# Performance work log

Hardware: AMD Instinct MI355X
Metric: run time of the kernel (lower is better)

The kernel has to match this reference:

```python
import jax, jax.numpy as jnp
import numpy as np

V, D, B, T, S, NH, DFF, NL, PAD = 4096, 512, 32, 32, 8, 8, 2048, 4, 0


def _ln(x, g, b, eps=1e-5):
    m = jnp.mean(x, -1, keepdims=True)
    v = jnp.mean((x - m) ** 2, -1, keepdims=True)
    return (x - m) * jax.lax.rsqrt(v + eps) * g + b


def _mha(q, k, v, in_w, in_b, out_w, out_b, attn_mask=None, kpm=None):
    b_, lq, d = q.shape
    lk = k.shape[1]
    dh = d // NH
    wq, wk, wv = jnp.split(in_w, 3, 0)
    bq, bk, bv = jnp.split(in_b, 3)
    qh = (q @ wq.T + bq).reshape(b_, lq, NH, dh).transpose(0, 2, 1, 3)
    kh = (k @ wk.T + bk).reshape(b_, lk, NH, dh).transpose(0, 2, 1, 3)
    vh = (v @ wv.T + bv).reshape(b_, lk, NH, dh).transpose(0, 2, 1, 3)
    s = jnp.einsum('bhqd,bhkd->bhqk', qh, kh) * (1.0 / np.sqrt(dh))
    if attn_mask is not None:
        s = jnp.where(attn_mask[None, None], -1e9, s)
    if kpm is not None:
        s = jnp.where(kpm[:, None, None, :], -1e9, s)
    a = jax.nn.softmax(s, -1)
    o = jnp.einsum('bhqk,bhkd->bhqd', a, vh).transpose(0, 2, 1, 3).reshape(b_, lq, d)
    return o @ out_w.T + out_b


def setup_inputs():
    key = jax.random.key(0)
    ks = iter(jax.random.split(key, 48))
    nrm = lambda shape, s=0.02: jax.random.normal(next(ks), shape, jnp.float32) * s
    d = {}
    d['input_ids'] = jax.random.randint(next(ks), (B, T), 1, V)
    d['ego_info'] = jax.random.normal(next(ks), (B, 3), jnp.float32)
    d['agent_tokens'] = jax.random.randint(next(ks), (B, T, S), 1, V)
    d['agent_feats'] = jax.random.normal(next(ks), (B, T, S, 5), jnp.float32)
    d['goal'] = jax.random.randint(next(ks), (B,), 1, V)
    d['emb'] = nrm((V, D), 1.0).at[PAD].set(0.0)  # padding_idx row zeroed
    d['se_w1'] = nrm((D, D + 3)); d['se_b1'] = jnp.zeros(D)
    d['se_w2'] = nrm((D, D)); d['se_b2'] = jnp.zeros(D)
    d['be_w1'] = nrm((D, D + 5)); d['be_b1'] = jnp.zeros(D)
    d['be_w2'] = nrm((D, D)); d['be_b2'] = jnp.zeros(D)
    for nm in ('in', 'mem', 'outn'):
        d[nm + '_g'] = jnp.ones(D); d[nm + '_b'] = jnp.zeros(D)
    d['sa_in_w'] = nrm((NL, 3 * D, D)); d['sa_in_b'] = jnp.zeros((NL, 3 * D))
    d['sa_out_w'] = nrm((NL, D, D)); d['sa_out_b'] = jnp.zeros((NL, D))
    d['ca_in_w'] = nrm((NL, 3 * D, D)); d['ca_in_b'] = jnp.zeros((NL, 3 * D))
    d['ca_out_w'] = nrm((NL, D, D)); d['ca_out_b'] = jnp.zeros((NL, D))
    d['ff_w1'] = nrm((NL, DFF, D)); d['ff_b1'] = jnp.zeros((NL, DFF))
    d['ff_w2'] = nrm((NL, D, DFF)); d['ff_b2'] = jnp.zeros((NL, D))
    for nm in ('ln1', 'ln2', 'ln3'):
        d[nm + '_g'] = jnp.ones((NL, D)); d[nm + '_b'] = jnp.zeros((NL, D))
    d['proj_w'] = nrm((V, D)); d['proj_b'] = jnp.zeros(V)
    return d


def _forward(input_ids, agent_tokens, goal, ego_info, agent_feats, emb, se_w1, se_b1, se_w2, se_b2, be_w1, be_b1, be_w2, be_b2, in_g, in_b, mem_g, mem_b, outn_g, outn_b, sa_in_w, sa_in_b, sa_out_w, sa_out_b, ca_in_w, ca_in_b, ca_out_w, ca_out_b, ff_w1, ff_b1, ff_w2, ff_b2, ln1_g, ln1_b, ln2_g, ln2_b, ln3_g, ln3_b, proj_w, proj_b):
    # --- encode_self_state: embed + fuse ego features -> (B, T, D) ---
    tok = emb[input_ids]
    ego = jnp.broadcast_to(ego_info[:, None, :], (B, T, 3))
    fused = jax.nn.relu(jnp.concatenate([tok, ego], -1) @ se_w1.T + se_b1) @ se_w2.T + se_b2
    self_state = _ln(fused, in_g, in_b)
    # --- encode_agent_topology -> env (B, T, S+1, D) ---
    amask = agent_tokens != -1
    aemb = emb[jnp.where(amask, agent_tokens, PAD)]
    astate = jax.nn.relu(jnp.concatenate([aemb, agent_feats], -1) @ be_w1.T + be_b1) @ be_w2.T + be_b2
    astate = astate * amask[..., None]
    goal_e = jnp.broadcast_to(emb[goal][:, None, None, :], (B, T, 1, D))
    env = _ln(jnp.concatenate([astate, goal_e], 2), mem_g, mem_b)
    # --- windowed memory for each step t in [1, T): frames [t-2, t-1, t] clipped ---
    steps = jnp.arange(1, T)
    idx = jnp.clip(steps[:, None] + jnp.array([-2, -1, 0]), 0, T - 1)  # (T-1, 3)
    mems = env[:, idx].reshape(B, T - 1, 3 * (S + 1), D).transpose(1, 0, 2, 3)  # (T-1, B, 3A, D)
    causal = jnp.triu(jnp.ones((T, T), bool), 1)
    kpm = input_ids == PAD

    # One full-length causal decoder run per step (vmapped); identical math to the
    # original prefix loop since position t only sees keys <= t, and we read position t.
    def decode(mem):
        x = self_state
        for l in range(NL):
            x = _ln(x + _mha(x, x, x, sa_in_w[l], sa_in_b[l], sa_out_w[l], sa_out_b[l], causal, kpm), ln1_g[l], ln1_b[l])
            x = _ln(x + _mha(x, mem, mem, ca_in_w[l], ca_in_b[l], ca_out_w[l], ca_out_b[l]), ln2_g[l], ln2_b[l])
            ff = jax.nn.relu(x @ ff_w1[l].T + ff_b1[l]) @ ff_w2[l].T + ff_b2[l]
            x = _ln(x + ff, ln3_g[l], ln3_b[l])
        return x

    dec_all = jax.vmap(decode)(mems)  # (T-1, B, T, D)
    sel = dec_all[jnp.arange(T - 1), :, steps, :]  # (T-1, B, D): last position of each prefix
    logits = _ln(sel, outn_g, outn_b) @ proj_w.T + proj_b
    return jnp.transpose(logits, (1, 0, 2))  # (B, T-1, V)


def reference(input_ids, ego_info, agent_tokens, agent_feats, goal, emb, se_w1, se_b1, se_w2, se_b2, be_w1, be_b1, be_w2, be_b2, in_g, in_b, mem_g, mem_b, outn_g, outn_b, sa_in_w, sa_in_b, sa_out_w, sa_out_b, ca_in_w, ca_in_b, ca_out_w, ca_out_b, ff_w1, ff_b1, ff_w2, ff_b2, ln1_g, ln1_b, ln2_g, ln2_b, ln3_g, ln3_b, proj_w, proj_b):
    return _forward(input_ids, agent_tokens, goal, ego_info, agent_feats, emb, se_w1, se_b1, se_w2, se_b2, be_w1, be_b1, be_w2, be_b2, in_g, in_b, mem_g, mem_b, outn_g, outn_b, sa_in_w, sa_in_b, sa_out_w, sa_out_b, ca_in_w, ca_in_b, ca_out_w, ca_out_b, ff_w1, ff_b1, ff_w2, ff_b2, ln1_g, ln1_b, ln2_g, ln2_b, ln3_g, ln3_b, proj_w, proj_b)
```

## Files before the change

### kernel.cpp

```cpp
#include <hip/hip_runtime.h>
#include <hip/hip_bf16.h>
#include <stdint.h>

typedef __hip_bfloat16 bf16;
typedef __attribute__((ext_vector_type(8))) short bf16x8;
typedef __attribute__((ext_vector_type(4))) float f32x4;

__device__ __forceinline__ float b2f(bf16 v) { return __bfloat162float(v); }
__device__ __forceinline__ bf16 f2b(float v) { return __float2bfloat16(v); }
__device__ __forceinline__ unsigned short f2bu(float v) {
    bf16 h = __float2bfloat16(v);
    return *(unsigned short*)&h;
}
__device__ __forceinline__ short f2bs(float v) {
    bf16 h = __float2bfloat16(v);
    return *(short*)&h;
}
__device__ __forceinline__ float su2f(unsigned short u) {
    unsigned int x = ((unsigned int)u) << 16;
    return *(float*)&x;
}

__device__ __forceinline__ void gload_lds16(const void* g, void* l) {
    __builtin_amdgcn_global_load_lds((const __attribute__((address_space(1))) void*)g,
                                     (__attribute__((address_space(3))) void*)l, 16, 0, 0);
}

__device__ __forceinline__ int swz_byte(int row, int kk) {
    return row * 80 + 2 * (kk & 7) + 16 * ((kk >> 3) ^ (row & 3));
}

__global__ __launch_bounds__(256) void mfma_gemm(
    const bf16* __restrict__ A, const bf16* __restrict__ W,
    const float* __restrict__ bias, void* __restrict__ C,
    int M, int N, int K, int c_bf16, int relu, int store_mode)
{
    __shared__ bf16 As[128 * 64];
    __shared__ bf16 Bs[128 * 64];
    const int gx = gridDim.x;
    const int nwg = gx * gridDim.y;
    const int orig = blockIdx.y * gx + blockIdx.x;
    const int qq = nwg >> 3, rr8 = nwg & 7;
    const int xcd = orig & 7, lid = orig >> 3;
    const int wgid = (xcd < rr8 ? xcd * (qq + 1) : rr8 * (qq + 1) + (xcd - rr8) * qq) + lid;
    const int m0 = (wgid / gx) * 128, n0 = (wgid % gx) * 128;

    const int tid = threadIdx.x;
    const int wave = tid >> 6, lane = tid & 63;
    const int wr = wave >> 1, wc = wave & 1;
    const int fr = lane & 15, fg = lane >> 4;
    f32x4 acc[4][4] = {};

    const int srow = lane >> 3;
    const int sunit = (lane & 7) ^ srow;

    for (int k0 = 0; k0 < K; k0 += 64) {
#pragma unroll
        for (int c = 0; c < 4; ++c) {
            const int chunk = wave * 4 + c;
            const int arow = m0 + chunk * 8 + srow;
            const int brow = n0 + chunk * 8 + srow;
            gload_lds16(A + (size_t)arow * K + k0 + sunit * 8, (char*)As + chunk * 1024);
            gload_lds16(W + (size_t)brow * K + k0 + sunit * 8, (char*)Bs + chunk * 1024);
        }
        __syncthreads();
#pragma unroll
        for (int kk = 0; kk < 64; kk += 32) {
            bf16x8 af[4], bw[4];
            const int bo = (kk + fg * 8) * 2;
#pragma unroll
            for (int t = 0; t < 4; ++t) {
                const int ra = wr * 64 + t * 16 + fr;
                af[t] = *(const bf16x8*)((const char*)As + ra * 128 + (bo ^ ((ra & 7) << 4)));
                const int rb = wc * 64 + t * 16 + fr;
                bw[t] = *(const bf16x8*)((const char*)Bs + rb * 128 + (bo ^ ((rb & 7) << 4)));
            }
#pragma unroll
            for (int mt = 0; mt < 4; ++mt)
#pragma unroll
                for (int nt = 0; nt < 4; ++nt)
                    acc[mt][nt] = __builtin_amdgcn_mfma_f32_16x16x32_bf16(
                        af[mt], bw[nt], acc[mt][nt], 0, 0, 0);
        }
        __syncthreads();
    }
#pragma unroll
    for (int mt = 0; mt < 4; ++mt) {
#pragma unroll
        for (int r = 0; r < 4; ++r) {
            const int m = m0 + wr * 64 + mt * 16 + fg * 4 + r;
            if (m >= M) continue;
            size_t orow = (size_t)m;
            if (store_mode == 1) orow = (size_t)(m & 31) * 31 + (m >> 5);
#pragma unroll
            for (int nt = 0; nt < 4; ++nt) {
                const int n = n0 + wc * 64 + nt * 16 + fr;
                float v = acc[mt][nt][r] + bias[n];
                if (relu) v = fmaxf(v, 0.f);
                if (c_bf16) ((bf16*)C)[orow * N + n] = f2b(v);
                else        ((float*)C)[orow * N + n] = v;
            }
        }
    }
}

__global__ __launch_bounds__(256) void self_attn_mfma(
    const bf16* __restrict__ qkv, const int* __restrict__ input_ids,
    bf16* __restrict__ attn_out)
{
    const int bid = blockIdx.x;
    const int hp = bid & 3;
    const int mb = bid >> 2;
    const int b = mb & 31;
    const size_t rowbase = (size_t)mb * 32;

    __shared__ __align__(16) char vt_raw[2][64 * 80];
    __shared__ __align__(16) char ps_raw[4][16 * 80];
    __shared__ float kpmv[32];

    const int tid = threadIdx.x;
    {
        const int r = tid & 31, u = tid >> 5;
#pragma unroll
        for (int e2 = 0; e2 < 2; ++e2) {
            const int h = hp * 2 + e2;
            bf16x8 v8 = *(const bf16x8*)(qkv + (rowbase + r) * 1536 + 1024 + h * 64 + u * 8);
#pragma unroll
            for (int j = 0; j < 8; ++j)
                *(short*)(vt_raw[e2] + swz_byte(u * 8 + j, r)) = v8[j];
        }
    }
    if (tid < 32) kpmv[tid] = (input_ids[b * 32 + tid] == 0) ? -1e9f : 0.f;
    __syncthreads();

    const int wave = tid >> 6, lane = tid & 63;
    const int e = wave >> 1;
    const int h = hp * 2 + e;
    const int qi = wave & 1;
    const int c = lane & 15, fg = lane >> 4;

    const bf16* qrow = qkv + (rowbase + qi * 16 + c) * 1536 + h * 64;
    bf16x8 af0 = *(const bf16x8*)(qrow + fg * 8);
    bf16x8 af1 = *(const bf16x8*)(qrow + 32 + fg * 8);
    f32x4 s[2];
#pragma unroll
    for (int kj = 0; kj < 2; ++kj) {
        const bf16* krow = qkv + (rowbase + kj * 16 + c) * 1536 + 512 + h * 64;
        bf16x8 b0 = *(const bf16x8*)(krow + fg * 8);
        bf16x8 b1 = *(const bf16x8*)(krow + 32 + fg * 8);
        f32x4 a = {};
        a = __builtin_amdgcn_mfma_f32_16x16x32_bf16(af0, b0, a, 0, 0, 0);
        a = __builtin_amdgcn_mfma_f32_16x16x32_bf16(af1, b1, a, 0, 0, 0);
        s[kj] = a;
    }

#pragma unroll
    for (int r = 0; r < 4; ++r) {
        const int qg = qi * 16 + fg * 4 + r;
        float v0 = s[0][r] * 0.125f + kpmv[c];
        float v1 = s[1][r] * 0.125f + kpmv[16 + c];
        if (c > qg) v0 = -1e9f;
        if (16 + c > qg) v1 = -1e9f;
        float m = fmaxf(v0, v1);
        m = fmaxf(m, __shfl_xor(m, 1)); m = fmaxf(m, __shfl_xor(m, 2));
        m = fmaxf(m, __shfl_xor(m, 4)); m = fmaxf(m, __shfl_xor(m, 8));
        float e0 = __expf(v0 - m), e1 = __expf(v1 - m);
        float sm = e0 + e1;
        sm += __shfl_xor(sm, 1); sm += __shfl_xor(sm, 2);
        sm += __shfl_xor(sm, 4); sm += __shfl_xor(sm, 8);
        float inv = 1.f / sm;
        *(short*)(ps_raw[wave] + swz_byte(fg * 4 + r, c))      = f2bs(e0 * inv);
        *(short*)(ps_raw[wave] + swz_byte(fg * 4 + r, 16 + c)) = f2bs(e1 * inv);
    }

    bf16x8 pa = *(const bf16x8*)(ps_raw[wave] + c * 80 + 16 * (fg ^ (c & 3)));
    f32x4 o[4];
#pragma unroll
    for (int dj = 0; dj < 4; ++dj) {
        bf16x8 bv = *(const bf16x8*)(vt_raw[e] + (dj * 16 + c) * 80 + 16 * (fg ^ (c & 3)));
        f32x4 a = {};
        o[dj] = __builtin_amdgcn_mfma_f32_16x16x32_bf16(pa, bv, a, 0, 0, 0);
    }
#pragma unroll
    for (int dj = 0; dj < 4; ++dj)
#pragma unroll
        for (int r = 0; r < 4; ++r)
            attn_out[(rowbase + qi * 16 + fg * 4 + r) * 512 + h * 64 + dj * 16 + c] = f2b(o[dj][r]);
}

__global__ __launch_bounds__(256) void cross_attn_mfma(
    const bf16* __restrict__ q, int qshared, const bf16* __restrict__ kv,
    bf16* __restrict__ attn_out)
{
    const int bid = blockIdx.x;
    const int hp = bid & 3;
    const int mb = bid >> 2;
    const size_t qb = (size_t)(qshared ? (mb & 31) : mb) * 32;
    const size_t kvb = (size_t)mb * 27;
    const size_t ob = (size_t)mb * 32;

    __shared__ __align__(16) char vt_raw[2][64 * 80];
    __shared__ __align__(16) char ps_raw[4][16 * 80];

    const int tid = threadIdx.x;
    {
        const int r = tid & 31, u = tid >> 5;
#pragma unroll
        for (int e2 = 0; e2 < 2; ++e2) {
            const int h = hp * 2 + e2;
            bf16x8 v8 = *(const bf16x8*)(kv + (kvb + r) * 1024 + 512 + h * 64 + u * 8);
#pragma unroll
            for (int j = 0; j < 8; ++j)
                *(short*)(vt_raw[e2] + swz_byte(u * 8 + j, r)) = v8[j];
        }
    }
    __syncthreads();

    const int wave = tid >> 6, lane = tid & 63;
    const int e = wave >> 1;
    const int h = hp * 2 + e;
    const int qi = wave & 1;
    const int c = lane & 15, fg = lane >> 4;

    const bf16* qrow = q + (qb + qi * 16 + c) * 512 + h * 64;
    bf16x8 af0 = *(const bf16x8*)(qrow + fg * 8);
    bf16x8 af1 = *(const bf16x8*)(qrow + 32 + fg * 8);
    f32x4 s[2];
#pragma unroll
    for (int kj = 0; kj < 2; ++kj) {
        const bf16* krow = kv + (kvb + kj * 16 + c) * 1024 + h * 64;
        bf16x8 b0 = *(const bf16x8*)(krow + fg * 8);
        bf16x8 b1 = *(const bf16x8*)(krow + 32 + fg * 8);
        f32x4 a = {};
        a = __builtin_amdgcn_mfma_f32_16x16x32_bf16(af0, b0, a, 0, 0, 0);
        a = __builtin_amdgcn_mfma_f32_16x16x32_bf16(af1, b1, a, 0, 0, 0);
        s[kj] = a;
    }
#pragma unroll
    for (int r = 0; r < 4; ++r) {
        float v0 = s[0][r] * 0.125f;
        float v1 = (16 + c < 27) ? s[1][r] * 0.125f : -1e9f;
        float m = fmaxf(v0, v1);
        m = fmaxf(m, __shfl_xor(m, 1)); m = fmaxf(m, __shfl_xor(m, 2));
        m = fmaxf(m, __shfl_xor(m, 4)); m = fmaxf(m, __shfl_xor(m, 8));
        float e0 = __expf(v0 - m), e1 = __expf(v1 - m);
        float sm = e0 + e1;
        sm += __shfl_xor(sm, 1); sm += __shfl_xor(sm, 2);
        sm += __shfl_xor(sm, 4); sm += __shfl_xor(sm, 8);
        float inv = 1.f / sm;
        *(short*)(ps_raw[wave] + swz_byte(fg * 4 + r, c))      = f2bs(e0 * inv);
        *(short*)(ps_raw[wave] + swz_byte(fg * 4 + r, 16 + c)) = f2bs(e1 * inv);
    }
    bf16x8 pa = *(const bf16x8*)(ps_raw[wave] + c * 80 + 16 * (fg ^ (c & 3)));
    f32x4 o[4];
#pragma unroll
    for (int dj = 0; dj < 4; ++dj) {
        bf16x8 bv = *(const bf16x8*)(vt_raw[e] + (dj * 16 + c) * 80 + 16 * (fg ^ (c & 3)));
        f32x4 a = {};
        o[dj] = __builtin_amdgcn_mfma_f32_16x16x32_bf16(pa, bv, a, 0, 0, 0);
    }
#pragma unroll
    for (int dj = 0; dj < 4; ++dj)
#pragma unroll
        for (int r = 0; r < 4; ++r)
            attn_out[(ob + qi * 16 + fg * 4 + r) * 512 + h * 64 + dj * 16 + c] = f2b(o[dj][r]);
}

__global__ __launch_bounds__(256) void ln_kernel(
    const float* __restrict__ x, const float* __restrict__ g,
    const float* __restrict__ b_, float* __restrict__ outf,
    bf16* __restrict__ outb, int rows)
{
    int row = blockIdx.x * 4 + (threadIdx.x >> 6);
    if (row >= rows) return;
    int lane = threadIdx.x & 63;
    const float4* xr = (const float4*)(x + (size_t)row * 512);
    float4 v[2];
    float sum = 0.f;
#pragma unroll
    for (int j = 0; j < 2; ++j) {
        v[j] = xr[lane + 64 * j];
        sum += v[j].x + v[j].y + v[j].z + v[j].w;
    }
    for (int o = 32; o; o >>= 1) sum += __shfl_xor(sum, o, 64);
    float mean = sum * (1.f / 512.f);
    float vs = 0.f;
#pragma unroll
    for (int j = 0; j < 2; ++j) {
        float dx = v[j].x - mean, dy = v[j].y - mean, dz = v[j].z - mean, dw = v[j].w - mean;
        vs += dx * dx + dy * dy + dz * dz + dw * dw;
    }
    for (int o = 32; o; o >>= 1) vs += __shfl_xor(vs, o, 64);
    float rstd = rsqrtf(vs * (1.f / 512.f) + 1e-5f);
#pragma unroll
    for (int j = 0; j < 2; ++j) {
        int u = lane + 64 * j;
        float4 g4 = ((const float4*)g)[u];
        float4 b4 = ((const float4*)b_)[u];
        float4 o4;
        o4.x = (v[j].x - mean) * rstd * g4.x + b4.x;
        o4.y = (v[j].y - mean) * rstd * g4.y + b4.y;
        o4.z = (v[j].z - mean) * rstd * g4.z + b4.z;
        o4.w = (v[j].w - mean) * rstd * g4.w + b4.w;
        if (outf) ((float4*)(outf + (size_t)row * 512))[u] = o4;
        if (outb) {
            ushort4 s4 = { f2bu(o4.x), f2bu(o4.y), f2bu(o4.z), f2bu(o4.w) };
            ((ushort4*)(outb + (size_t)row * 512))[u] = s4;
        }
    }
}

__global__ __launch_bounds__(256) void ln_res2_kernel(
    const float* __restrict__ xin, int rowmask, const bf16* __restrict__ br,
    const float* __restrict__ g, const float* __restrict__ b_,
    float* __restrict__ xout, bf16* __restrict__ xbout, int rows)
{
    int row = blockIdx.x * 4 + (threadIdx.x >> 6);
    if (row >= rows) return;
    int lane = threadIdx.x & 63;
    const float4* xr = (const float4*)(xin + (size_t)(row & rowmask) * 512);
    const ushort4* brr = (const ushort4*)(br + (size_t)row * 512);
    float4 v[2];
    float sum = 0.f;
#pragma unroll
    for (int j = 0; j < 2; ++j) {
        int u = lane + 64 * j;
        float4 a = xr[u];
        ushort4 s4 = brr[u];
        a.x += su2f(s4.x); a.y += su2f(s4.y); a.z += su2f(s4.z); a.w += su2f(s4.w);
        v[j] = a;
        sum += a.x + a.y + a.z + a.w;
    }
    for (int o = 32; o; o >>= 1) sum += __shfl_xor(sum, o, 64);
    float mean = sum * (1.f / 512.f);
    float vs = 0.f;
#pragma unroll
    for (int j = 0; j < 2; ++j) {
        float dx = v[j].x - mean, dy = v[j].y - mean, dz = v[j].z - mean, dw = v[j].w - mean;
        vs += dx * dx + dy * dy + dz * dz + dw * dw;
    }
    for (int o = 32; o; o >>= 1) vs += __shfl_xor(vs, o, 64);
    float rstd = rsqrtf(vs * (1.f / 512.f) + 1e-5f);
#pragma unroll
    for (int j = 0; j < 2; ++j) {
        int u = lane + 64 * j;
        float4 g4 = ((const float4*)g)[u];
        float4 b4 = ((const float4*)b_)[u];
        float4 o4;
        o4.x = (v[j].x - mean) * rstd * g4.x + b4.x;
        o4.y = (v[j].y - mean) * rstd * g4.y + b4.y;
        o4.z = (v[j].z - mean) * rstd * g4.z + b4.z;
        o4.w = (v[j].w - mean) * rstd * g4.w + b4.w;
        ((float4*)(xout + (size_t)row * 512))[u] = o4;
        ushort4 s4 = { f2bu(o4.x), f2bu(o4.y), f2bu(o4.z), f2bu(o4.w) };
        ((ushort4*)(xbout + (size_t)row * 512))[u] = s4;
    }
}

__global__ __launch_bounds__(256) void env_ln_kernel(
    const float* __restrict__ astate, const int* __restrict__ atok,
    const float* __restrict__ emb, const int* __restrict__ goal,
    const float* __restrict__ g, const float* __restrict__ b_, float* __restrict__ env)
{
    int row = blockIdx.x * 4 + (threadIdx.x >> 6);
    if (row >= 9216) return;
    int lane = threadIdx.x & 63;
    int s9 = row % 9;
    int bt = row / 9;
    float4 v[2];
    if (s9 < 8) {
        int ar = bt * 8 + s9;
        float msk = (atok[ar] != -1) ? 1.f : 0.f;
#pragma unroll
        for (int j = 0; j < 2; ++j) {
            float4 a = ((const float4*)(astate + (size_t)ar * 512))[lane + 64 * j];
            a.x *= msk; a.y *= msk; a.z *= msk; a.w *= msk;
            v[j] = a;
        }
    } else {
        int gi = goal[bt >> 5];
#pragma unroll
        for (int j = 0; j < 2; ++j)
            v[j] = ((const float4*)(emb + (size_t)gi * 512))[lane + 64 * j];
    }
    float sum = 0.f;
#pragma unroll
    for (int j = 0; j < 2; ++j) sum += v[j].x + v[j].y + v[j].z + v[j].w;
    for (int o = 32; o; o >>= 1) sum += __shfl_xor(sum, o, 64);
    float mean = sum * (1.f / 512.f);
    float vs = 0.f;
#pragma unroll
    for (int j = 0; j < 2; ++j) {
        float dx = v[j].x - mean, dy = v[j].y - mean, dz = v[j].z - mean, dw = v[j].w - mean;
        vs += dx * dx + dy * dy + dz * dz + dw * dw;
    }
    for (int o = 32; o; o >>= 1) vs += __shfl_xor(vs, o, 64);
    float rstd = rsqrtf(vs * (1.f / 512.f) + 1e-5f);
#pragma unroll
    for (int j = 0; j < 2; ++j) {
        int u = lane + 64 * j;
        float4 g4 = ((const float4*)g)[u];
        float4 b4 = ((const float4*)b_)[u];
        float4 o4;
        o4.x = (v[j].x - mean) * rstd * g4.x + b4.x;
        o4.y = (v[j].y - mean) * rstd * g4.y + b4.y;
        o4.z = (v[j].z - mean) * rstd * g4.z + b4.z;
        o4.w = (v[j].w - mean) * rstd * g4.w + b4.w;
        ((float4*)(env + (size_t)row * 512))[u] = o4;
    }
}

__global__ void mems_kernel(const float* __restrict__ env, bf16* __restrict__ mems)
{
    int row = blockIdx.x;
    int j = row % 27;
    int mb = row / 27;
    int m = mb >> 5, b = mb & 31;
    int gidx = j / 9, sp = j % 9;
    int t = m - 1 + gidx;
    t = t < 0 ? 0 : (t > 31 ? 31 : t);
    const float4* src = (const float4*)(env + ((size_t)(b * 32 + t) * 9 + sp) * 512);
    ushort4* dst = (ushort4*)(mems + (size_t)row * 512);
    int tid = threadIdx.x;
#pragma unroll
    for (int k = 0; k < 2; ++k) {
        int u = tid + 64 * k;
        float4 a = src[u];
        ushort4 s4 = { f2bu(a.x), f2bu(a.y), f2bu(a.z), f2bu(a.w) };
        dst[u] = s4;
    }
}

__global__ void xcatb_kernel(const int* __restrict__ ids, const float* __restrict__ ego,
                             const bf16* __restrict__ emb_b, bf16* __restrict__ xcat)
{
    int row = blockIdx.x;
    int tid = threadIdx.x;
    int b = row >> 5;
    int id = ids[row];
    bf16x8* dst = (bf16x8*)(xcat + (size_t)row * 576);
    if (tid < 64) {
        dst[tid] = ((const bf16x8*)(emb_b + (size_t)id * 512))[tid];
    } else if (tid == 64) {
        bf16x8 u = {};
        u[0] = f2bs(ego[b * 3 + 0]);
        u[1] = f2bs(ego[b * 3 + 1]);
        u[2] = f2bs(ego[b * 3 + 2]);
        dst[64] = u;
    } else if (tid < 72) {
        bf16x8 z = {};
        dst[tid] = z;
    }
}

__global__ void acatb_kernel(const int* __restrict__ atok, const float* __restrict__ afeat,
                             const bf16* __restrict__ emb_b, bf16* __restrict__ acat)
{
    int row = blockIdx.x;
    int tid = threadIdx.x;
    int tok = atok[row];
    int id = (tok != -1) ? tok : 0;
    bf16x8* dst = (bf16x8*)(acat + (size_t)row * 576);
    if (tid < 64) {
        dst[tid] = ((const bf16x8*)(emb_b + (size_t)id * 512))[tid];
    } else if (tid == 64) {
        bf16x8 u = {};
#pragma unroll
        for (int e = 0; e < 5; ++e) u[e] = f2bs(afeat[(size_t)row * 5 + e]);
        dst[64] = u;
    } else if (tid < 72) {
        bf16x8 z = {};
        dst[tid] = z;
    }
}

__global__ void sel_kernel(const float* __restrict__ x, float* __restrict__ sel, int m0, int cm)
{
    int row = blockIdx.x;
    int ml = row >> 5, b = row & 31;
    int m = m0 + ml;
    const float4* src = (const float4*)(x + ((size_t)(ml * 32 + b) * 32 + (m + 1)) * 512);
    float4* dst = (float4*)(sel + ((size_t)m * 32 + b) * 512);
    dst[threadIdx.x] = src[threadIdx.x];
}

__global__ void fill_kernel(float* __restrict__ o, int n, float v)
{
    int i = blockIdx.x * 256 + threadIdx.x;
    if (i < n) o[i] = v;
}

__global__ void cvtw_kernel(const float* __restrict__ s, unsigned short* __restrict__ d, int n)
{
    int n4 = n >> 2;
    int stride = gridDim.x * blockDim.x;
    for (int i = blockIdx.x * blockDim.x + threadIdx.x; i < n4; i += stride) {
        float4 v = ((const float4*)s)[i];
        ushort4 u = { f2bu(v.x), f2bu(v.y), f2bu(v.z), f2bu(v.w) };
        ((ushort4*)d)[i] = u;
    }
}

__global__ void cvtpad_kernel(const float* __restrict__ s, bf16* __restrict__ d, int Ks)
{
    int row = blockIdx.x;
    int tid = threadIdx.x;
    for (int c = tid; c < 576; c += 256) {
        float v = (c < Ks) ? s[(size_t)row * Ks + c] : 0.f;
        d[(size_t)row * 576 + c] = f2b(v);
    }
}

extern "C" void kernel_launch(void* const* d_in, const int* in_sizes, int n_in,
                              void* d_out, int out_size, void* d_ws, size_t ws_size,
                              hipStream_t stream)
{
    float* out = (float*)d_out;
    if (n_in < 40) {
        fill_kernel<<<(out_size + 255) / 256, 256, 0, stream>>>(out, out_size, 1e6f);
        return;
    }
    const int*   input_ids = (const int*)d_in[0];
    const float* ego       = (const float*)d_in[1];
    const int*   atok      = (const int*)d_in[2];
    const float* afeat     = (const float*)d_in[3];
    const int*   goal      = (const int*)d_in[4];
    const float* emb       = (const float*)d_in[5];
    const float* se_w1 = (const float*)d_in[6];
    const float* se_b1 = (const float*)d_in[7];
    const float* se_w2 = (const float*)d_in[8];
    const float* se_b2 = (const float*)d_in[9];
    const float* be_w1 = (const float*)d_in[10];
    const float* be_b1 = (const float*)d_in[11];
    const float* be_w2 = (const float*)d_in[12];
    const float* be_b2 = (const float*)d_in[13];
    const float* in_g  = (const float*)d_in[14];
    const float* in_b  = (const float*)d_in[15];
    const float* mem_g = (const float*)d_in[16];
    const float* mem_b = (const float*)d_in[17];
    const float* outn_g = (const float*)d_in[18];
    const float* outn_b = (const float*)d_in[19];
    const float* sa_in_w  = (const float*)d_in[20];
    const float* sa_in_b  = (const float*)d_in[21];
    const float* sa_out_w = (const float*)d_in[22];
    const float* sa_out_b = (const float*)d_in[23];
    const float* ca_in_w  = (const float*)d_in[24];
    const float* ca_in_b  = (const float*)d_in[25];
    const float* ca_out_w = (const float*)d_in[26];
    const float* ca_out_b = (const float*)d_in[27];
    const float* ff_w1 = (const float*)d_in[28];
    const float* ff_b1 = (const float*)d_in[29];
    const float* ff_w2 = (const float*)d_in[30];
    const float* ff_b2 = (const float*)d_in[31];
    const float* ln1_g = (const float*)d_in[32];
    const float* ln1_b = (const float*)d_in[33];
    const float* ln2_g = (const float*)d_in[34];
    const float* ln2_b = (const float*)d_in[35];
    const float* ln3_g = (const float*)d_in[36];
    const float* ln3_b = (const float*)d_in[37];
    const float* proj_w = (const float*)d_in[38];
    const float* proj_b = (const float*)d_in[39];

    auto ALIGN = [](size_t b) { return (b + 255) & ~(size_t)255; };
    uintptr_t base = (uintptr_t)d_ws;
    uintptr_t cur = (base + 255) & ~(uintptr_t)255;
    auto alloc = [&](size_t bytes) -> char* {
        char* r = (char*)cur; cur += (bytes + 255) & ~(size_t)255; return r;
    };

    float* self_state = (float*)alloc((size_t)1024 * 512 * 4);
    bf16*  ss_b       = (bf16*) alloc((size_t)1024 * 512 * 2);
    float* x0         = (float*)alloc((size_t)1024 * 512 * 4);
    bf16*  xb0        = (bf16*) alloc((size_t)1024 * 512 * 2);
    bf16*  q0b        = (bf16*) alloc((size_t)1024 * 512 * 2);
    bf16*  qkv0       = (bf16*) alloc((size_t)1024 * 1536 * 2);
    bf16*  araw0      = (bf16*) alloc((size_t)1024 * 512 * 2);
    bf16*  brnch0     = (bf16*) alloc((size_t)1024 * 512 * 2);
    bf16*  mems       = (bf16*) alloc((size_t)(26784 + 128) * 512 * 2);
    float* sel        = (float*)alloc((size_t)1024 * 512 * 4);
    bf16*  sel_ln_b   = (bf16*) alloc((size_t)1024 * 512 * 2);
    bf16* w_emb   = (bf16*)alloc((size_t)4096 * 512 * 2);
    bf16* w_se1p  = (bf16*)alloc((size_t)512 * 576 * 2);
    bf16* w_be1p  = (bf16*)alloc((size_t)512 * 576 * 2);
    bf16* w_se2   = (bf16*)alloc((size_t)512 * 512 * 2);
    bf16* w_be2   = (bf16*)alloc((size_t)512 * 512 * 2);
    bf16* w_sain  = (bf16*)alloc((size_t)4 * 1536 * 512 * 2);
    bf16* w_saout = (bf16*)alloc((size_t)4 * 512 * 512 * 2);
    bf16* w_cain  = (bf16*)alloc((size_t)4 * 1536 * 512 * 2);
    bf16* w_caout = (bf16*)alloc((size_t)4 * 512 * 512 * 2);
    bf16* w_ff1   = (bf16*)alloc((size_t)4 * 2048 * 512 * 2);
    bf16* w_ff2   = (bf16*)alloc((size_t)4 * 2048 * 512 * 2);
    bf16* w_proj  = (bf16*)alloc((size_t)4096 * 512 * 2);
    uintptr_t big = cur;

    size_t setup_need =
        ALIGN((size_t)1024 * 576 * 2) + ALIGN((size_t)1024 * 512 * 2) + ALIGN((size_t)1024 * 512 * 4) +
        ALIGN((size_t)8192 * 576 * 2) + ALIGN((size_t)8192 * 512 * 2) + ALIGN((size_t)8192 * 512 * 4) +
        ALIGN((size_t)9216 * 512 * 4);
    auto chunk_need = [&](int c) -> size_t {
        return ALIGN((size_t)c * 1024 * 512 * 4)
             + ALIGN((size_t)c * 1024 * 512 * 2)
             + ALIGN((size_t)c * 1024 * 1536 * 2)
             + ALIGN((size_t)c * 1024 * 512 * 2)
             + ALIGN((size_t)c * 1024 * 512 * 2)
             + ALIGN((size_t)c * 1024 * 2048 * 2)
             + ALIGN(((size_t)c * 864 + 128) * 1024 * 2);
    };
    int CH = 0;
    if (ws_size > (size_t)(big - base) + 4096) {
        size_t avail = ws_size - (size_t)(big - base) - 4096;
        for (int c = 31; c >= 1; --c)
            if (setup_need <= avail && chunk_need(c) <= avail) { CH = c; break; }
    }
    if (!CH) {
        fill_kernel<<<(out_size + 255) / 256, 256, 0, stream>>>(out, out_size, 1e6f);
        return;
    }

    auto cvt = [&](const float* s, bf16* d, size_t n) {
        int n4 = (int)(n >> 2);
        int blocks = (n4 + 255) / 256; if (blocks > 2048) blocks = 2048;
        cvtw_kernel<<<blocks, 256, 0, stream>>>(s, (unsigned short*)d, (int)n);
    };
    cvt(emb, w_emb, (size_t)4096 * 512);
    cvtpad_kernel<<<512, 256, 0, stream>>>(se_w1, w_se1p, 515);
    cvtpad_kernel<<<512, 256, 0, stream>>>(be_w1, w_be1p, 517);
    cvt(se_w2, w_se2, (size_t)512 * 512);
    cvt(be_w2, w_be2, (size_t)512 * 512);
    cvt(sa_in_w, w_sain, (size_t)4 * 1536 * 512);
    cvt(sa_out_w, w_saout, (size_t)4 * 512 * 512);
    cvt(ca_in_w, w_cain, (size_t)4 * 1536 * 512);
    cvt(ca_out_w, w_caout, (size_t)4 * 512 * 512);
    cvt(ff_w1, w_ff1, (size_t)4 * 2048 * 512);
    cvt(ff_w2, w_ff2, (size_t)4 * 2048 * 512);
    cvt(proj_w, w_proj, (size_t)4096 * 512);

    auto launch_mfma = [&](const bf16* A, const bf16* W, const float* bias,
                           void* C, int c_bf16, int M, int N, int K, int relu, int smode) {
        dim3 g(N / 128, (M + 127) / 128);
        mfma_gemm<<<g, 256, 0, stream>>>(A, W, bias, C, M, N, K, c_bf16, relu, smode);
    };

    {
        uintptr_t sp = big;
        auto salloc = [&](size_t b) -> char* { char* r = (char*)sp; sp += ALIGN(b); return r; };
        bf16*  xcat_b = (bf16*) salloc((size_t)1024 * 576 * 2);
        bf16*  h1b    = (bf16*) salloc((size_t)1024 * 512 * 2);
        float* fused  = (float*)salloc((size_t)1024 * 512 * 4);
        bf16*  acat_b = (bf16*) salloc((size_t)8192 * 576 * 2);
        bf16*  ah1b   = (bf16*) salloc((size_t)8192 * 512 * 2);
        float* astate = (float*)salloc((size_t)8192 * 512 * 4);
        float* env    = (float*)salloc((size_t)9216 * 512 * 4);

        xcatb_kernel<<<1024, 128, 0, stream>>>(input_ids, ego, w_emb, xcat_b);
        launch_mfma(xcat_b, w_se1p, se_b1, h1b, 1, 1024, 512, 576, 1, 0);
        launch_mfma(h1b, w_se2, se_b2, fused, 0, 1024, 512, 512, 0, 0);
        ln_kernel<<<256, 256, 0, stream>>>(fused, in_g, in_b, self_state, ss_b, 1024);

        acatb_kernel<<<8192, 128, 0, stream>>>(atok, afeat, w_emb, acat_b);
        launch_mfma(acat_b, w_be1p, be_b1, ah1b, 1, 8192, 512, 576, 1, 0);
        launch_mfma(ah1b, w_be2, be_b2, astate, 0, 8192, 512, 512, 0, 0);
        env_ln_kernel<<<2304, 256, 0, stream>>>(astate, atok, emb, goal, mem_g, mem_b, env);
        mems_kernel<<<26784, 64, 0, stream>>>(env, mems);
    }

    launch_mfma(ss_b, w_sain, sa_in_b, qkv0, 1, 1024, 1536, 512, 0, 0);
    self_attn_mfma<<<32 * 4, 256, 0, stream>>>(qkv0, input_ids, araw0);
    launch_mfma(araw0, w_saout, sa_out_b, brnch0, 1, 1024, 512, 512, 0, 0);
    ln_res2_kernel<<<256, 256, 0, stream>>>(self_state, 0x7fffffff, brnch0,
                                            ln1_g, ln1_b, x0, xb0, 1024);
    launch_mfma(xb0, w_cain, ca_in_b, q0b, 1, 1024, 512, 512, 0, 0);

    {
        uintptr_t sp = big;
        auto salloc = [&](size_t b) -> char* { char* r = (char*)sp; sp += ALIGN(b); return r; };
        float* x     = (float*)salloc((size_t)CH * 1024 * 512 * 4);
        bf16*  xb    = (bf16*) salloc((size_t)CH * 1024 * 512 * 2);
        bf16*  qkv   = (bf16*) salloc((size_t)CH * 1024 * 1536 * 2);
        bf16*  araw  = (bf16*) salloc((size_t)CH * 1024 * 512 * 2);
        bf16*  brnch = (bf16*) salloc((size_t)CH * 1024 * 512 * 2);
        bf16*  ff1b  = (bf16*) salloc((size_t)CH * 1024 * 2048 * 2);
        bf16*  kv    = (bf16*) salloc(((size_t)CH * 864 + 128) * 1024 * 2);

        for (int m0 = 0; m0 < 31; m0 += CH) {
            int cm = (31 - m0) < CH ? (31 - m0) : CH;
            int Mr = cm * 1024;
            launch_mfma(mems + (size_t)m0 * 864 * 512, w_cain + (size_t)512 * 512,
                        ca_in_b + 512, kv, 1, cm * 864, 1024, 512, 0, 0);
            cross_attn_mfma<<<cm * 32 * 4, 256, 0, stream>>>(q0b, 1, kv, araw);
            launch_mfma(araw, w_caout, ca_out_b, brnch, 1, Mr, 512, 512, 0, 0);
            ln_res2_kernel<<<(Mr + 3) / 4, 256, 0, stream>>>(x0, 1023, brnch,
                                                             ln2_g, ln2_b, x, xb, Mr);
            launch_mfma(xb, w_ff1, ff_b1, ff1b, 1, Mr, 2048, 512, 1, 0);
            launch_mfma(ff1b, w_ff2, ff_b2, brnch, 1, Mr, 512, 2048, 0, 0);
            ln_res2_kernel<<<(Mr + 3) / 4, 256, 0, stream>>>(x, 0x7fffffff, brnch,
                                                             ln3_g, ln3_b, x, xb, Mr);
            for (int l = 1; l < 4; ++l) {
                launch_mfma(xb, w_sain + (size_t)l * 1536 * 512, sa_in_b + l * 1536,
                            qkv, 1, Mr, 1536, 512, 0, 0);
                self_attn_mfma<<<cm * 32 * 4, 256, 0, stream>>>(qkv, input_ids, araw);
                launch_mfma(araw, w_saout + (size_t)l * 512 * 512, sa_out_b + l * 512,
                            brnch, 1, Mr, 512, 512, 0, 0);
                ln_res2_kernel<<<(Mr + 3) / 4, 256, 0, stream>>>(x, 0x7fffffff, brnch,
                                                                 ln1_g + l * 512, ln1_b + l * 512, x, xb, Mr);
                launch_mfma(xb, w_cain + (size_t)l * 1536 * 512, ca_in_b + l * 1536,
                            qkv, 1, Mr, 512, 512, 0, 0);
                launch_mfma(mems + (size_t)m0 * 864 * 512,
                            w_cain + (size_t)l * 1536 * 512 + (size_t)512 * 512,
                            ca_in_b + l * 1536 + 512,
                            kv, 1, cm * 864, 1024, 512, 0, 0);
                cross_attn_mfma<<<cm * 32 * 4, 256, 0, stream>>>(qkv, 0, kv, araw);
                launch_mfma(araw, w_caout + (size_t)l * 512 * 512, ca_out_b + l * 512,
                            brnch, 1, Mr, 512, 512, 0, 0);
                ln_res2_kernel<<<(Mr + 3) / 4, 256, 0, stream>>>(x, 0x7fffffff, brnch,
                                                                 ln2_g + l * 512, ln2_b + l * 512, x, xb, Mr);
                launch_mfma(xb, w_ff1 + (size_t)l * 2048 * 512, ff_b1 + l * 2048,
                            ff1b, 1, Mr, 2048, 512, 1, 0);
                launch_mfma(ff1b, w_ff2 + (size_t)l * 512 * 2048, ff_b2 + l * 512,
                            brnch, 1, Mr, 512, 2048, 0, 0);
                ln_res2_kernel<<<(Mr + 3) / 4, 256, 0, stream>>>(x, 0x7fffffff, brnch,
                                                                 ln3_g + l * 512, ln3_b + l * 512, x, xb, Mr);
            }
            sel_kernel<<<cm * 32, 128, 0, stream>>>(x, sel, m0, cm);
        }
    }

    ln_kernel<<<248, 256, 0, stream>>>(sel, outn_g, outn_b, (float*)nullptr, sel_ln_b, 992);
    launch_mfma(sel_ln_b, w_proj, proj_b, out, 0, 992, 4096, 512, 0, 1);
}
```

Baseline: 3.446 ms.

## Project cross-attention K/V once per unique env row and gather by index

Result: slower. 3.823 ms (+10.9%).

```diff
diff --git a/kernel.cpp b/kernel.cpp
--- a/kernel.cpp
+++ b/kernel.cpp
@@ -153,7 +153,6 @@
         a = __builtin_amdgcn_mfma_f32_16x16x32_bf16(af1, b1, a, 0, 0, 0);
         s[kj] = a;
     }
-
 #pragma unroll
     for (int r = 0; r < 4; ++r) {
         const int qg = qi * 16 + fg * 4 + r;
@@ -172,7 +171,6 @@
         *(short*)(ps_raw[wave] + swz_byte(fg * 4 + r, c))      = f2bs(e0 * inv);
         *(short*)(ps_raw[wave] + swz_byte(fg * 4 + r, 16 + c)) = f2bs(e1 * inv);
     }
-
     bf16x8 pa = *(const bf16x8*)(ps_raw[wave] + c * 80 + 16 * (fg ^ (c & 3)));
     f32x4 o[4];
 #pragma unroll
@@ -188,15 +186,23 @@
             attn_out[(rowbase + qi * 16 + fg * 4 + r) * 512 + h * 64 + dj * 16 + c] = f2b(o[dj][r]);
 }
 
+__device__ __forceinline__ int env_idx(int m, int b, int j) {
+    int gi = j / 9, sp = j - gi * 9;
+    int t = m - 1 + gi;
+    t = t < 0 ? 0 : (t > 31 ? 31 : t);
+    return (b * 32 + t) * 9 + sp;
+}
+
 __global__ __launch_bounds__(256) void cross_attn_mfma(
-    const bf16* __restrict__ q, int qshared, const bf16* __restrict__ kv,
-    bf16* __restrict__ attn_out)
+    const bf16* __restrict__ q, int qshared, const bf16* __restrict__ ekv,
+    bf16* __restrict__ attn_out, int m0glob)
 {
     const int bid = blockIdx.x;
     const int hp = bid & 3;
     const int mb = bid >> 2;
-    const size_t qb = (size_t)(qshared ? (mb & 31) : mb) * 32;
-    const size_t kvb = (size_t)mb * 27;
+    const int b = mb & 31;
+    const int m = m0glob + (mb >> 5);
+    const size_t qb = (size_t)(qshared ? b : mb) * 32;
     const size_t ob = (size_t)mb * 32;
 
     __shared__ __align__(16) char vt_raw[2][64 * 80];
@@ -205,10 +211,11 @@
     const int tid = threadIdx.x;
     {
         const int r = tid & 31, u = tid >> 5;
+        const size_t erow = (size_t)env_idx(m, b, r) * 1024;
 #pragma unroll
         for (int e2 = 0; e2 < 2; ++e2) {
             const int h = hp * 2 + e2;
-            bf16x8 v8 = *(const bf16x8*)(kv + (kvb + r) * 1024 + 512 + h * 64 + u * 8);
+            bf16x8 v8 = *(const bf16x8*)(ekv + erow + 512 + h * 64 + u * 8);
 #pragma unroll
             for (int j = 0; j < 8; ++j)
                 *(short*)(vt_raw[e2] + swz_byte(u * 8 + j, r)) = v8[j];
@@ -228,9 +235,9 @@
     f32x4 s[2];
 #pragma unroll
     for (int kj = 0; kj < 2; ++kj) {
-        const bf16* krow = kv + (kvb + kj * 16 + c) * 1024 + h * 64;
-        bf16x8 b0 = *(const bf16x8*)(krow + fg * 8);
-        bf16x8 b1 = *(const bf16x8*)(krow + 32 + fg * 8);
+        const size_t erow = (size_t)env_idx(m, b, kj * 16 + c) * 1024;
+        bf16x8 b0 = *(const bf16x8*)(ekv + erow + h * 64 + fg * 8);
+        bf16x8 b1 = *(const bf16x8*)(ekv + erow + h * 64 + 32 + fg * 8);
         f32x4 a = {};
         a = __builtin_amdgcn_mfma_f32_16x16x32_bf16(af0, b0, a, 0, 0, 0);
         a = __builtin_amdgcn_mfma_f32_16x16x32_bf16(af1, b1, a, 0, 0, 0);
@@ -240,10 +247,10 @@
     for (int r = 0; r < 4; ++r) {
         float v0 = s[0][r] * 0.125f;
         float v1 = (16 + c < 27) ? s[1][r] * 0.125f : -1e9f;
-        float m = fmaxf(v0, v1);
-        m = fmaxf(m, __shfl_xor(m, 1)); m = fmaxf(m, __shfl_xor(m, 2));
-        m = fmaxf(m, __shfl_xor(m, 4)); m = fmaxf(m, __shfl_xor(m, 8));
-        float e0 = __expf(v0 - m), e1 = __expf(v1 - m);
+        float m2 = fmaxf(v0, v1);
+        m2 = fmaxf(m2, __shfl_xor(m2, 1)); m2 = fmaxf(m2, __shfl_xor(m2, 2));
+        m2 = fmaxf(m2, __shfl_xor(m2, 4)); m2 = fmaxf(m2, __shfl_xor(m2, 8));
+        float e0 = __expf(v0 - m2), e1 = __expf(v1 - m2);
         float sm = e0 + e1;
         sm += __shfl_xor(sm, 1); sm += __shfl_xor(sm, 2);
         sm += __shfl_xor(sm, 4); sm += __shfl_xor(sm, 8);
@@ -360,7 +367,7 @@
 __global__ __launch_bounds__(256) void env_ln_kernel(
     const float* __restrict__ astate, const int* __restrict__ atok,
     const float* __restrict__ emb, const int* __restrict__ goal,
-    const float* __restrict__ g, const float* __restrict__ b_, float* __restrict__ env)
+    const float* __restrict__ g, const float* __restrict__ b_, bf16* __restrict__ envb)
 {
     int row = blockIdx.x * 4 + (threadIdx.x >> 6);
     if (row >= 9216) return;
@@ -401,33 +408,12 @@
         int u = lane + 64 * j;
         float4 g4 = ((const float4*)g)[u];
         float4 b4 = ((const float4*)b_)[u];
-        float4 o4;
-        o4.x = (v[j].x - mean) * rstd * g4.x + b4.x;
-        o4.y = (v[j].y - mean) * rstd * g4.y + b4.y;
-        o4.z = (v[j].z - mean) * rstd * g4.z + b4.z;
-        o4.w = (v[j].w - mean) * rstd * g4.w + b4.w;
-        ((float4*)(env + (size_t)row * 512))[u] = o4;
-    }
-}
-
-__global__ void mems_kernel(const float* __restrict__ env, bf16* __restrict__ mems)
-{
-    int row = blockIdx.x;
-    int j = row % 27;
-    int mb = row / 27;
-    int m = mb >> 5, b = mb & 31;
-    int gidx = j / 9, sp = j % 9;
-    int t = m - 1 + gidx;
-    t = t < 0 ? 0 : (t > 31 ? 31 : t);
-    const float4* src = (const float4*)(env + ((size_t)(b * 32 + t) * 9 + sp) * 512);
-    ushort4* dst = (ushort4*)(mems + (size_t)row * 512);
-    int tid = threadIdx.x;
-#pragma unroll
-    for (int k = 0; k < 2; ++k) {
-        int u = tid + 64 * k;
-        float4 a = src[u];
-        ushort4 s4 = { f2bu(a.x), f2bu(a.y), f2bu(a.z), f2bu(a.w) };
-        dst[u] = s4;
+        ushort4 s4;
+        s4.x = f2bu((v[j].x - mean) * rstd * g4.x + b4.x);
+        s4.y = f2bu((v[j].y - mean) * rstd * g4.y + b4.y);
+        s4.z = f2bu((v[j].z - mean) * rstd * g4.z + b4.z);
+        s4.w = f2bu((v[j].w - mean) * rstd * g4.w + b4.w);
+        ((ushort4*)(envb + (size_t)row * 512))[u] = s4;
     }
 }
 
@@ -576,7 +562,8 @@
     bf16*  qkv0       = (bf16*) alloc((size_t)1024 * 1536 * 2);
     bf16*  araw0      = (bf16*) alloc((size_t)1024 * 512 * 2);
     bf16*  brnch0     = (bf16*) alloc((size_t)1024 * 512 * 2);
-    bf16*  mems       = (bf16*) alloc((size_t)(26784 + 128) * 512 * 2);
+    bf16*  env_b      = (bf16*) alloc((size_t)9216 * 512 * 2);
+    bf16*  env_kv     = (bf16*) alloc((size_t)4 * 9216 * 1024 * 2);
     float* sel        = (float*)alloc((size_t)1024 * 512 * 4);
     bf16*  sel_ln_b   = (bf16*) alloc((size_t)1024 * 512 * 2);
     bf16* w_emb   = (bf16*)alloc((size_t)4096 * 512 * 2);
@@ -594,17 +581,17 @@
     uintptr_t big = cur;
 
     size_t setup_need =
-        ALIGN((size_t)1024 * 576 * 2) + ALIGN((size_t)1024 * 512 * 2) + ALIGN((size_t)1024 * 512 * 4) +
-        ALIGN((size_t)8192 * 576 * 2) + ALIGN((size_t)8192 * 512 * 2) + ALIGN((size_t)8192 * 512 * 4) +
-        ALIGN((size_t)9216 * 512 * 4);
+        ALIGN((size_t)1024 * 576 * 2) + ALIGN((size_t)1024 * 512 * 2) +
+        ALIGN((size_t)1024 * 512 * 4) +
+        ALIGN((size_t)8192 * 576 * 2) + ALIGN((size_t)8192 * 512 * 2) +
+        ALIGN((size_t)8192 * 512 * 4);
     auto chunk_need = [&](int c) -> size_t {
         return ALIGN((size_t)c * 1024 * 512 * 4)
              + ALIGN((size_t)c * 1024 * 512 * 2)
              + ALIGN((size_t)c * 1024 * 1536 * 2)
              + ALIGN((size_t)c * 1024 * 512 * 2)
              + ALIGN((size_t)c * 1024 * 512 * 2)
-             + ALIGN((size_t)c * 1024 * 2048 * 2)
-             + ALIGN(((size_t)c * 864 + 128) * 1024 * 2);
+             + ALIGN((size_t)c * 1024 * 2048 * 2);
     };
     int CH = 0;
     if (ws_size > (size_t)(big - base) + 4096) {
@@ -650,7 +637,6 @@
         bf16*  acat_b = (bf16*) salloc((size_t)8192 * 576 * 2);
         bf16*  ah1b   = (bf16*) salloc((size_t)8192 * 512 * 2);
         float* astate = (float*)salloc((size_t)8192 * 512 * 4);
-        float* env    = (float*)salloc((size_t)9216 * 512 * 4);
 
         xcatb_kernel<<<1024, 128, 0, stream>>>(input_ids, ego, w_emb, xcat_b);
         launch_mfma(xcat_b, w_se1p, se_b1, h1b, 1, 1024, 512, 576, 1, 0);
@@ -660,9 +646,12 @@
         acatb_kernel<<<8192, 128, 0, stream>>>(atok, afeat, w_emb, acat_b);
         launch_mfma(acat_b, w_be1p, be_b1, ah1b, 1, 8192, 512, 576, 1, 0);
         launch_mfma(ah1b, w_be2, be_b2, astate, 0, 8192, 512, 512, 0, 0);
-        env_ln_kernel<<<2304, 256, 0, stream>>>(astate, atok, emb, goal, mem_g, mem_b, env);
-        mems_kernel<<<26784, 64, 0, stream>>>(env, mems);
-    }
+        env_ln_kernel<<<2304, 256, 0, stream>>>(astate, atok, emb, goal, mem_g, mem_b, env_b);
+    }
+    for (int l = 0; l < 4; ++l)
+        launch_mfma(env_b, w_cain + (size_t)l * 1536 * 512 + (size_t)512 * 512,
+                    ca_in_b + l * 1536 + 512,
+                    env_kv + (size_t)l * 9216 * 1024, 1, 9216, 1024, 512, 0, 0);
 
     launch_mfma(ss_b, w_sain, sa_in_b, qkv0, 1, 1024, 1536, 512, 0, 0);
     self_attn_mfma<<<32 * 4, 256, 0, stream>>>(qkv0, input_ids, araw0);
@@ -680,14 +669,11 @@
         bf16*  araw  = (bf16*) salloc((size_t)CH * 1024 * 512 * 2);
         bf16*  brnch = (bf16*) salloc((size_t)CH * 1024 * 512 * 2);
         bf16*  ff1b  = (bf16*) salloc((size_t)CH * 1024 * 2048 * 2);
-        bf16*  kv    = (bf16*) salloc(((size_t)CH * 864 + 128) * 1024 * 2);
 
         for (int m0 = 0; m0 < 31; m0 += CH) {
             int cm = (31 - m0) < CH ? (31 - m0) : CH;
             int Mr = cm * 1024;
-            launch_mfma(mems + (size_t)m0 * 864 * 512, w_cain + (size_t)512 * 512,
-                        ca_in_b + 512, kv, 1, cm * 864, 1024, 512, 0, 0);
-            cross_attn_mfma<<<cm * 32 * 4, 256, 0, stream>>>(q0b, 1, kv, araw);
+            cross_attn_mfma<<<cm * 32 * 4, 256, 0, stream>>>(q0b, 1, env_kv, araw, m0);
             launch_mfma(araw, w_caout, ca_out_b, brnch, 1, Mr, 512, 512, 0, 0);
             ln_res2_kernel<<<(Mr + 3) / 4, 256, 0, stream>>>(x0, 1023, brnch,
                                                              ln2_g, ln2_b, x, xb, Mr);
@@ -705,11 +691,8 @@
                                                                  ln1_g + l * 512, ln1_b + l * 512, x, xb, Mr);
                 launch_mfma(xb, w_cain + (size_t)l * 1536 * 512, ca_in_b + l * 1536,
                             qkv, 1, Mr, 512, 512, 0, 0);
-                launch_mfma(mems + (size_t)m0 * 864 * 512,
-                            w_cain + (size_t)l * 1536 * 512 + (size_t)512 * 512,
-                            ca_in_b + l * 1536 + 512,
-                            kv, 1, cm * 864, 1024, 512, 0, 0);
-                cross_attn_mfma<<<cm * 32 * 4, 256, 0, stream>>>(qkv, 0, kv, araw);
+                cross_attn_mfma<<<cm * 32 * 4, 256, 0, stream>>>(
+                    qkv, 0, env_kv + (size_t)l * 9216 * 1024, araw, m0);
                 launch_mfma(araw, w_caout + (size_t)l * 512 * 512, ca_out_b + l * 512,
                             brnch, 1, Mr, 512, 512, 0, 0);
                 ln_res2_kernel<<<(Mr + 3) / 4, 256, 0, stream>>>(x, 0x7fffffff, brnch,
```
